# Performance work log

Hardware: AMD Instinct MI355X
Metric: run time of the kernel (lower is better)

The kernel has to match this reference:

```python
import jax, jax.numpy as jnp
import numpy as np

N_NODES = 50000
N_EDGES = 800000
N_GRAPHS = 64
NEG_SLOPE = 0.2  # PyG GATv2Conv default negative_slope
LN_EPS = 1e-5


def gatv2(x, src, dst, Wl, bl, Wr, br, att, bias, heads, out_ch, concat):
    """Faithful eval-mode PyG GATv2Conv: x_l=lin_l(x) (source), x_r=lin_r(x) (target),
    e = att . leaky_relu(x_l[src] + x_r[dst]), segment-softmax over dst, scatter-add."""
    N = x.shape[0]
    H, C = heads, out_ch
    xl = (x @ Wl + bl).reshape(N, H, C)
    xr = (x @ Wr + br).reshape(N, H, C)
    e = jax.nn.leaky_relu(xl[src] + xr[dst], NEG_SLOPE)        # [E, H, C]
    logits = jnp.einsum('ehc,hc->eh', e, att)                  # [E, H]
    m = jax.ops.segment_max(logits, dst, num_segments=N)       # every node has a self-loop
    ex = jnp.exp(logits - m[dst])
    denom = jax.ops.segment_sum(ex, dst, num_segments=N)
    alpha = ex / (denom[dst] + 1e-16)                          # [E, H]
    out = jax.ops.segment_sum(xl[src] * alpha[..., None], dst, num_segments=N)  # [N, H, C]
    out = out.reshape(N, H * C) if concat else out.mean(axis=1)
    return out + bias


def setup_inputs() -> dict:
    key = jax.random.key(0)
    ks = jax.random.split(key, 32)

    def g(i, shape):  # glorot-ish
        scale = np.sqrt(2.0 / (shape[0] + shape[-1]))
        return (jax.random.normal(ks[i], shape, jnp.float32) * scale)

    inp = {
        'x': jax.random.normal(ks[0], (N_NODES, 4), jnp.float32),
        'edge_index': jax.random.randint(ks[1], (2, N_EDGES), 0, N_NODES, dtype=jnp.int64),
        'batch': jnp.sort(jax.random.randint(ks[2], (N_NODES,), 0, N_GRAPHS, dtype=jnp.int64)),
        # conv1: 4 -> 64, heads=4, concat -> 256
        'W1l': g(3, (4, 256)), 'b1l': jnp.zeros((256,), jnp.float32),
        'W1r': g(4, (4, 256)), 'b1r': jnp.zeros((256,), jnp.float32),
        'a1': g(5, (4, 64)), 'c1b': jnp.zeros((256,), jnp.float32),
        # conv2: 256 -> 64, heads=2, concat -> 128
        'W2l': g(6, (256, 128)), 'b2l': jnp.zeros((128,), jnp.float32),
        'W2r': g(7, (256, 128)), 'b2r': jnp.zeros((128,), jnp.float32),
        'a2': g(8, (2, 64)), 'c2b': jnp.zeros((128,), jnp.float32),
        # conv3: 128 -> 256, heads=1, concat=False -> 256
        'W3l': g(9, (128, 256)), 'b3l': jnp.zeros((256,), jnp.float32),
        'W3r': g(10, (128, 256)), 'b3r': jnp.zeros((256,), jnp.float32),
        'a3': g(11, (1, 256)), 'c3b': jnp.zeros((256,), jnp.float32),
        # enhancer MLP + LayerNorm
        'We1': g(12, (256, 512)), 'be1': jnp.zeros((512,), jnp.float32),
        'We2': g(13, (512, 256)), 'be2': jnp.zeros((256,), jnp.float32),
        'lng': jnp.ones((256,), jnp.float32), 'lnb': jnp.zeros((256,), jnp.float32),
    }
    return inp


def reference(x, edge_index, batch,
              W1l, b1l, W1r, b1r, a1, c1b,
              W2l, b2l, W2r, b2r, a2, c2b,
              W3l, b3l, W3r, b3r, a3, c3b,
              We1, be1, We2, be2, lng, lnb):
    N = x.shape[0]
    loop = jnp.arange(N, dtype=edge_index.dtype)  # add_self_loops=True (PyG default)
    src = jnp.concatenate([edge_index[0], loop])
    dst = jnp.concatenate([edge_index[1], loop])

    h = jax.nn.relu(gatv2(x, src, dst, W1l, b1l, W1r, b1r, a1, c1b, 4, 64, True))
    h = jax.nn.relu(gatv2(h, src, dst, W2l, b2l, W2r, b2r, a2, c2b, 2, 64, True))
    h = gatv2(h, src, dst, W3l, b3l, W3r, b3r, a3, c3b, 1, 256, False)

    # global mean pool per graph
    sums = jax.ops.segment_sum(h, batch, num_segments=N_GRAPHS)          # [G, 256]
    cnt = jax.ops.segment_sum(jnp.ones((N, 1), h.dtype), batch, num_segments=N_GRAPHS)
    pooled = sums / jnp.maximum(cnt, 1.0)

    # enhancer (dropout off in eval): Linear -> ReLU -> Linear -> LayerNorm
    z = jax.nn.relu(pooled @ We1 + be1) @ We2 + be2
    mu = z.mean(axis=-1, keepdims=True)
    var = z.var(axis=-1, keepdims=True)
    return (z - mu) / jnp.sqrt(var + LN_EPS) * lng + lnb
```

## Files before the change

kernel.cpp:

```cpp
#include <hip/hip_runtime.h>
#include <hip/hip_bf16.h>
#include <math.h>

#define NN 50000
#define NE0 800000
#define ETOT (NE0 + NN)
#define NG 64
#define SCAN_BLKS ((NN + 63) / 64)
#define DMAX_THR 8.0f

typedef _Float16 h2 __attribute__((ext_vector_type(2)));
typedef _Float16 h8 __attribute__((ext_vector_type(8)));
typedef float    f32x4 __attribute__((ext_vector_type(4)));
typedef unsigned short us8 __attribute__((ext_vector_type(8)));

__device__ __forceinline__ unsigned short f2h(float f) {
    _Float16 h = (_Float16)f;
    return __builtin_bit_cast(unsigned short, h);
}
__device__ __forceinline__ float h2f(unsigned short u) {
    return (float)__builtin_bit_cast(_Float16, u);
}

__device__ __forceinline__ void edge_sd(const int* __restrict__ ei, int e, int& s, int& d) {
    if (e < NE0) { s = ei[e]; d = ei[NE0 + e]; }
    else { s = e - NE0; d = s; }
}

__global__ __launch_bounds__(256)
void hist_dst(const int* __restrict__ ei, int* __restrict__ deg) {
    int e = blockIdx.x * blockDim.x + threadIdx.x;
    if (e >= ETOT) return;
    int s, d; edge_sd(ei, e, s, d); (void)s;
    atomicAdd(&deg[d], 1);
}

__global__ __launch_bounds__(64)
void scan1(const int* __restrict__ deg, int* __restrict__ psum) {
    int i = blockIdx.x * 64 + threadIdx.x;
    int v = (i < NN) ? deg[i] : 0;
#pragma unroll
    for (int off = 1; off < 64; off <<= 1) {
        int t = __shfl_up(v, off);
        if ((int)threadIdx.x >= off) v += t;
    }
    if (threadIdx.x == 63) psum[blockIdx.x] = v;
}

__global__ __launch_bounds__(1024)
void scan2(int* __restrict__ psum) {
    __shared__ int sm[1024];
    int t = threadIdx.x;
    sm[t] = (t < SCAN_BLKS) ? psum[t] : 0;
    __syncthreads();
    for (int off = 1; off < 1024; off <<= 1) {
        int v = (t >= off) ? sm[t - off] : 0;
        __syncthreads();
        sm[t] += v;
        __syncthreads();
    }
    if (t < SCAN_BLKS) psum[t] = (t == 0) ? 0 : sm[t - 1];
}

__global__ __launch_bounds__(64)
void scan3(const int* __restrict__ deg, const int* __restrict__ psum,
           int* __restrict__ rowptr, int* __restrict__ cursor) {
    int i = blockIdx.x * 64 + threadIdx.x;
    int v = (i < NN) ? deg[i] : 0;
    int inc = v;
#pragma unroll
    for (int off = 1; off < 64; off <<= 1) {
        int t = __shfl_up(inc, off);
        if ((int)threadIdx.x >= off) inc += t;
    }
    int excl = inc - v + psum[blockIdx.x];
    if (i < NN) { rowptr[i] = excl; cursor[i] = excl; }
    if (i == NN - 1) rowptr[NN] = excl + v;
}

__global__ __launch_bounds__(256)
void scatter_csr(const int* __restrict__ ei, int* __restrict__ cursor,
                 int* __restrict__ col) {
    int e = blockIdx.x * blockDim.x + threadIdx.x;
    if (e >= ETOT) return;
    int s, d; edge_sd(ei, e, s, d);
    int pos = atomicAdd(&cursor[d], 1);
    col[pos] = s;
}

__device__ __forceinline__ void wfrag_one(const float* W, unsigned short* Wf,
                                          int r, int KB, int NOUT) {
    int j = r & 7;
    int l = (r >> 3) & 63;
    int rest = r >> 9;
    int kb = rest % KB, t = rest / KB;
    int k = kb * 32 + (l >> 4) * 8 + j;
    int colj = t * 16 + (l & 15);
    Wf[r] = f2h(W[(size_t)k * NOUT + colj]);
}
__global__ __launch_bounds__(256)
void wfrag_all(const float* __restrict__ W2l, const float* __restrict__ W2r,
               const float* __restrict__ W3l, const float* __restrict__ W3r,
               unsigned short* __restrict__ Wf2l, unsigned short* __restrict__ Wf2r,
               unsigned short* __restrict__ Wf3l, unsigned short* __restrict__ Wf3r,
               int* __restrict__ deg) {
    int tid = blockIdx.x * 256 + threadIdx.x;
    if (tid < NN) deg[tid] = 0;
    int seg = tid >> 15;
    int r = tid & 32767;
    if (seg == 0)      wfrag_one(W2l, Wf2l, r, 8, 128);
    else if (seg == 1) wfrag_one(W2r, Wf2r, r, 8, 128);
    else if (seg == 2) wfrag_one(W3l, Wf3l, r, 4, 256);
    else               wfrag_one(W3r, Wf3r, r, 4, 256);
}

__global__ __launch_bounds__(256)
void qr_prep(const float* __restrict__ X,
             const float* __restrict__ W1l, const float* __restrict__ b1l,
             const float* __restrict__ W1r, const float* __restrict__ b1r,
             unsigned short* __restrict__ Q, unsigned short* __restrict__ R) {
    int j = blockIdx.x * 64 + (threadIdx.x & 63);
    int row0 = (blockIdx.y * 4 + (threadIdx.x >> 6)) * 8;
    float l0 = W1l[j], l1 = W1l[256 + j], l2 = W1l[512 + j], l3 = W1l[768 + j];
    float r0 = W1r[j], r1 = W1r[256 + j], r2 = W1r[512 + j], r3 = W1r[768 + j];
    float bl = b1l[j], br = b1r[j];
#pragma unroll
    for (int r = 0; r < 8; ++r) {
        int row = row0 + r;
        if (row >= NN) break;
        float4 xv = *reinterpret_cast<const float4*>(X + (size_t)row * 4);
        float q = fmaf(xv.x, l0, fmaf(xv.y, l1, fmaf(xv.z, l2, fmaf(xv.w, l3, bl))));
        float rr = fmaf(xv.x, r0, fmaf(xv.y, r1, fmaf(xv.z, r2, fmaf(xv.w, r3, br))));
        Q[(size_t)row * 256 + j] = f2h(q);
        R[(size_t)row * 256 + j] = f2h(rr);
    }
}

template<int CPL, int REDW, bool RELU>
__global__ __launch_bounds__(256)
void gat_fused(const unsigned short* __restrict__ xl, const unsigned short* __restrict__ xr,
               const int* __restrict__ rowptr, const int* __restrict__ col,
               const float* __restrict__ att, const float* __restrict__ bias,
               unsigned short* __restrict__ out) {
    constexpr int HC = CPL * 32;
    constexpr int NP = CPL / 2;
    int lane = threadIdx.x & 63;
    int half = lane >> 5;
    int node = (blockIdx.x * blockDim.x + threadIdx.x) >> 6;
    if (node >= NN) return;
    int ch0 = (lane & 31) * CPL;

    const h2 c02 = (h2){(_Float16)0.2f, (_Float16)0.2f};
    h2 a2[NP];
#pragma unroll
    for (int p = 0; p < NP; ++p)
        a2[p] = (h2){(_Float16)att[ch0 + 2*p], (_Float16)att[ch0 + 2*p + 1]};
    h2 r2[NP];
    {
        const h2* rp = reinterpret_cast<const h2*>(xr + (size_t)node * HC + ch0);
#pragma unroll
        for (int p = 0; p < NP; ++p) r2[p] = rp[p];
    }

    float m = -INFINITY, l = 0.f, acc[CPL];
#pragma unroll
    for (int p = 0; p < CPL; ++p) acc[p] = 0.f;

    int beg = rowptr[node], end = rowptr[node + 1];
    int n = end - beg;
    int nh = (n + 1) >> 1;
    int idx = beg + (half ? nh : 0);
    int myEnd = half ? end : beg + nh;

    for (; idx + 3 < myEnd; idx += 4) {
        int s[4] = { col[idx], col[idx + 1], col[idx + 2], col[idx + 3] };
        h2 e[4][NP];
#pragma unroll
        for (int q = 0; q < 4; ++q) {
            const h2* pq = reinterpret_cast<const h2*>(xl + (size_t)s[q] * HC + ch0);
#pragma unroll
            for (int p = 0; p < NP; ++p) e[q][p] = pq[p];
        }
        float d[4] = { 0.f, 0.f, 0.f, 0.f };
#pragma unroll
        for (int p = 0; p < NP; ++p) {
#pragma unroll
            for (int q = 0; q < 4; ++q) {
                h2 u = e[q][p] + r2[p];
                u = __builtin_elementwise_max(u, u * c02);
                d[q] = __builtin_amdgcn_fdot2(u, a2[p], d[q], false);
            }
        }
#pragma unroll
        for (int off = REDW >> 1; off >= 1; off >>= 1) {
#pragma unroll
            for (int q = 0; q < 4; ++q) d[q] += __shfl_xor(d[q], off);
        }
        float pmax = fmaxf(fmaxf(d[0], d[1]), fmaxf(d[2], d[3]));
        if (pmax > m + DMAX_THR) {
            float sc = __expf(m - pmax);
            l *= sc;
#pragma unroll
            for (int p = 0; p < CPL; ++p) acc[p] *= sc;
            m = pmax;
        }
        float pw[4];
#pragma unroll
        for (int q = 0; q < 4; ++q) pw[q] = __expf(d[q] - m);
        l += (pw[0] + pw[1]) + (pw[2] + pw[3]);
#pragma unroll
        for (int p = 0; p < CPL; ++p) {
            float t0 = fmaf(pw[0], (float)e[0][p >> 1][p & 1],
                            pw[1] * (float)e[1][p >> 1][p & 1]);
            float t1 = fmaf(pw[2], (float)e[2][p >> 1][p & 1],
                            pw[3] * (float)e[3][p >> 1][p & 1]);
            acc[p] += t0 + t1;
        }
    }
    for (; idx < myEnd; ++idx) {
        int s0 = col[idx];
        const h2* p0 = reinterpret_cast<const h2*>(xl + (size_t)s0 * HC + ch0);
        h2 e0[NP];
#pragma unroll
        for (int p = 0; p < NP; ++p) e0[p] = p0[p];
        float d0 = 0.f;
#pragma unroll
        for (int p = 0; p < NP; ++p) {
            h2 u0 = e0[p] + r2[p];
            u0 = __builtin_elementwise_max(u0, u0 * c02);
            d0 = __builtin_amdgcn_fdot2(u0, a2[p], d0, false);
        }
#pragma unroll
        for (int off = REDW >> 1; off >= 1; off >>= 1) d0 += __shfl_xor(d0, off);
        if (d0 > m + DMAX_THR) {
            float sc = __expf(m - d0);
            l *= sc;
#pragma unroll
            for (int p = 0; p < CPL; ++p) acc[p] *= sc;
            m = d0;
        }
        float pw0 = __expf(d0 - m);
        l += pw0;
#pragma unroll
        for (int p = 0; p < CPL; ++p)
            acc[p] = fmaf(pw0, (float)e0[p >> 1][p & 1], acc[p]);
    }

    float mo = __shfl_xor(m, 32);
    float lo = __shfl_xor(l, 32);
    float M = fmaxf(m, mo);
    float sA = __expf(m - M), sB = __expf(mo - M);
    float lsum = l * sA + lo * sB;
    float inv = 1.f / (lsum + 1e-16f);
    unsigned short o[CPL];
#pragma unroll
    for (int p = 0; p < CPL; ++p) {
        float ao = __shfl_xor(acc[p], 32);
        float v = (acc[p] * sA + ao * sB) * inv + bias[ch0 + p];
        if (RELU) v = fmaxf(v, 0.f);
        o[p] = f2h(v);
    }
    if (half == 0) {
        if constexpr (CPL == 8) {
            us8 ov;
#pragma unroll
            for (int p = 0; p < 8; ++p) ov[p] = o[p];
            *reinterpret_cast<us8*>(out + (size_t)node * HC + ch0) = ov;
        } else {
            *reinterpret_cast<ushort4*>(out + (size_t)node * HC + ch0) =
                make_ushort4(o[0], o[1], o[2], o[3]);
        }
    }
}

template<int KIN, int NOUT>
__global__ __launch_bounds__(256)
void gemm_mfma2(const unsigned short* __restrict__ X,
                const unsigned short* __restrict__ WfL, const float* __restrict__ bL,
                unsigned short* __restrict__ outL,
                const unsigned short* __restrict__ WfR, const float* __restrict__ bR,
                unsigned short* __restrict__ outR) {
    constexpr int KB = KIN / 32, NT = NOUT / 16;
    int lane = threadIdx.x & 63;
    int wv = threadIdx.x >> 6;
    int row0 = blockIdx.x * 64 + wv * 16;
    int r16 = lane & 15, kg = lane >> 4;

    int arow = row0 + r16; if (arow >= NN) arow = NN - 1;
    const unsigned short* xrow = X + (size_t)arow * KIN + kg * 8;
    h8 af[KB];
#pragma unroll
    for (int kb = 0; kb < KB; ++kb)
        af[kb] = *reinterpret_cast<const h8*>(xrow + kb * 32);

    const unsigned short* Wf[2] = { WfL, WfR };
    const float* bb[2] = { bL, bR };
    unsigned short* oo[2] = { outL, outR };

#pragma unroll
    for (int w = 0; w < 2; ++w) {
        const h8* wbase = reinterpret_cast<const h8*>(Wf[w]) + lane;
        const float* bw = bb[w];
        unsigned short* ow = oo[w];
#pragma unroll 1
        for (int t = 0; t < NT; ++t) {
            f32x4 acc = {0.f, 0.f, 0.f, 0.f};
            const h8* wp = wbase + (size_t)t * KB * 64;
#pragma unroll
            for (int kb = 0; kb < KB; ++kb)
                acc = __builtin_amdgcn_mfma_f32_16x16x32_f16(af[kb], wp[kb * 64], acc, 0, 0, 0);
            float bv = bw[t * 16 + r16];
#pragma unroll
            for (int rg = 0; rg < 4; ++rg) {
                int row = row0 + kg * 4 + rg;
                if (row < NN)
                    ow[(size_t)row * NOUT + t * 16 + r16] = f2h(acc[rg] + bv);
            }
        }
    }
}

__global__ __launch_bounds__(256)
void graph_bounds(const int* __restrict__ batch, float* __restrict__ cnt,
                  float* __restrict__ pooled) {
    int g = blockIdx.x, tid = threadIdx.x;
    pooled[g * 256 + tid] = 0.f;
    if (tid == 0) {
        int lo = 0, hi = NN;
        while (lo < hi) { int mid = (lo + hi) >> 1; if (batch[mid] < g) lo = mid + 1; else hi = mid; }
        int lo2 = lo, hi2 = NN;
        while (lo2 < hi2) { int mid = (lo2 + hi2) >> 1; if (batch[mid] < g + 1) lo2 = mid + 1; else hi2 = mid; }
        cnt[g] = (float)(lo2 - lo);
    }
}

__global__ __launch_bounds__(256)
void pool_sum(const unsigned short* __restrict__ h, const int* __restrict__ batch,
              float* pooled) {
    __shared__ int gb[32];
    int c = threadIdx.x;
    int n0 = blockIdx.x * 32;
    int n1 = min(n0 + 32, NN);
    int cnt = n1 - n0;
    if (c < cnt) gb[c] = batch[n0 + c];
    __syncthreads();
    if (gb[0] == gb[cnt - 1]) {
        float acc = 0.f;
#pragma unroll 4
        for (int i = 0; i < cnt; ++i) acc += h2f(h[(size_t)(n0 + i) * 256 + c]);
        atomicAdd(&pooled[gb[0] * 256 + c], acc);
    } else {
        int cur = gb[0]; float acc = 0.f;
        for (int i = 0; i < cnt; ++i) {
            int g = gb[i];
            if (g != cur) { atomicAdd(&pooled[cur * 256 + c], acc); acc = 0.f; cur = g; }
            acc += h2f(h[(size_t)(n0 + i) * 256 + c]);
        }
        atomicAdd(&pooled[cur * 256 + c], acc);
    }
}

__global__ __launch_bounds__(256)
void mlp_ln(const float* __restrict__ pooled, const float* __restrict__ cnt,
            const float* __restrict__ We1, const float* __restrict__ be1,
            const float* __restrict__ We2, const float* __restrict__ be2,
            const float* __restrict__ lng, const float* __restrict__ lnb,
            float* __restrict__ out) {
    __shared__ float p[256];
    __shared__ float t[512];
    __shared__ float red[8];
    int g = blockIdx.x, tid = threadIdx.x;
    p[tid] = pooled[g * 256 + tid] / fmaxf(cnt[g], 1.0f);
    __syncthreads();
    for (int jj = tid; jj < 512; jj += 256) {
        float s = be1[jj];
        for (int k = 0; k < 256; ++k) s = fmaf(p[k], We1[(size_t)k * 512 + jj], s);
        t[jj] = fmaxf(s, 0.f);
    }
    __syncthreads();
    float z = be2[tid];
    for (int k = 0; k < 512; ++k) z = fmaf(t[k], We2[(size_t)k * 256 + tid], z);
    float sv = z, sq = z * z;
#pragma unroll
    for (int off = 32; off >= 1; off >>= 1) {
        sv += __shfl_xor(sv, off);
        sq += __shfl_xor(sq, off);
    }
    int wv = tid >> 6;
    if ((tid & 63) == 0) { red[wv] = sv; red[4 + wv] = sq; }
    __syncthreads();
    float tot = red[0] + red[1] + red[2] + red[3];
    float totq = red[4] + red[5] + red[6] + red[7];
    float mu = tot * (1.f / 256.f);
    float var = totq * (1.f / 256.f) - mu * mu;
    float r = rsqrtf(var + 1e-5f);
    out[g * 256 + tid] = (z - mu) * r * lng[tid] + lnb[tid];
}

extern "C" void kernel_launch(void* const* d_in, const int* in_sizes, int n_in,
                              void* d_out, int out_size, void* d_ws, size_t ws_size,
                              hipStream_t stream) {
    const float* x   = (const float*)d_in[0];
    const int*   ei  = (const int*)d_in[1];
    const int*   bat = (const int*)d_in[2];
    const float *W1l = (const float*)d_in[3], *b1l = (const float*)d_in[4];
    const float *W1r = (const float*)d_in[5], *b1r = (const float*)d_in[6];
    const float *a1  = (const float*)d_in[7], *c1b = (const float*)d_in[8];
    const float *W2l = (const float*)d_in[9],  *b2l = (const float*)d_in[10];
    const float *W2r = (const float*)d_in[11], *b2r = (const float*)d_in[12];
    const float *a2  = (const float*)d_in[13], *c2b = (const float*)d_in[14];
    const float *W3l = (const float*)d_in[15], *b3l = (const float*)d_in[16];
    const float *W3r = (const float*)d_in[17], *b3r = (const float*)d_in[18];
    const float *a3  = (const float*)d_in[19], *c3b = (const float*)d_in[20];
    const float *We1 = (const float*)d_in[21], *be1 = (const float*)d_in[22];
    const float *We2 = (const float*)d_in[23], *be2 = (const float*)d_in[24];
    const float *lng = (const float*)d_in[25], *lnb = (const float*)d_in[26];

    char* base = (char*)d_ws;
    size_t off = 0;
    auto nxt = [&](size_t bytes) { char* p = base + off; off = (off + bytes + 255) & ~(size_t)255; return p; };
    unsigned short* Abuf = (unsigned short*)nxt((size_t)NN * 256 * 2);
    unsigned short* Bbuf = (unsigned short*)nxt((size_t)NN * 256 * 2);
    unsigned short* Hb16 = (unsigned short*)nxt((size_t)NN * 256 * 2);
    unsigned short* Qtab = (unsigned short*)nxt((size_t)NN * 256 * 2);
    unsigned short* Rtab = (unsigned short*)nxt((size_t)NN * 256 * 2);
    int* deg    = (int*)nxt(NN * 4);
    int* rowptr = (int*)nxt((NN + 1) * 4);
    int* cursor = (int*)nxt(NN * 4);
    int* colv   = (int*)nxt((size_t)ETOT * 4);
    int* psum   = (int*)nxt(1024 * 4);
    float* POOL = (float*)nxt(NG * 256 * 4);
    float* CNT  = (float*)nxt(NG * 4);
    unsigned short* Wf2l = (unsigned short*)nxt(256 * 128 * 2);
    unsigned short* Wf2r = (unsigned short*)nxt(256 * 128 * 2);
    unsigned short* Wf3l = (unsigned short*)nxt(128 * 256 * 2);
    unsigned short* Wf3r = (unsigned short*)nxt(128 * 256 * 2);

    const int GEMM_BLKS = (NN + 63) / 64;
    const int NB_NODE = (NN + 3) / 4;

    wfrag_all<<<(4 * 32768) / 256, 256, 0, stream>>>(W2l, W2r, W3l, W3r,
                                                     Wf2l, Wf2r, Wf3l, Wf3r, deg);
    hist_dst<<<(ETOT + 255) / 256, 256, 0, stream>>>(ei, deg);
    scan1<<<SCAN_BLKS, 64, 0, stream>>>(deg, psum);
    scan2<<<1, 1024, 0, stream>>>(psum);
    scan3<<<SCAN_BLKS, 64, 0, stream>>>(deg, psum, rowptr, cursor);
    scatter_csr<<<(ETOT + 255) / 256, 256, 0, stream>>>(ei, cursor, colv);

    {
        dim3 g(4, (NN + 31) / 32);
        qr_prep<<<g, 256, 0, stream>>>(x, W1l, b1l, W1r, b1r, Qtab, Rtab);
    }

    gat_fused<8, 8, true><<<NB_NODE, 256, 0, stream>>>(Qtab, Rtab, rowptr, colv, a1, c1b, Hb16);

    gemm_mfma2<256, 128><<<GEMM_BLKS, 256, 0, stream>>>(Hb16, Wf2l, b2l, Abuf, Wf2r, b2r, Bbuf);
    gat_fused<4, 16, true><<<NB_NODE, 256, 0, stream>>>(Abuf, Bbuf, rowptr, colv, a2, c2b, Hb16);

    gemm_mfma2<128, 256><<<GEMM_BLKS, 256, 0, stream>>>(Hb16, Wf3l, b3l, Abuf, Wf3r, b3r, Bbuf);
    gat_fused<8, 32, false><<<NB_NODE, 256, 0, stream>>>(Abuf, Bbuf, rowptr, colv, a3, c3b, Hb16);

    graph_bounds<<<NG, 256, 0, stream>>>(bat, CNT, POOL);
    pool_sum<<<(NN + 31) / 32, 256, 0, stream>>>(Hb16, bat, POOL);
    mlp_ln<<<NG, 256, 0, stream>>>(POOL, CNT, We1, be1, We2, be2, lng, lnb, (float*)d_out);
}
```

Measured before the change: 413.4 us.

## Accumulate GAT messages in packed fp16 and generalize edge split per node

The fused GAT kernel now keeps the weighted-message accumulator in packed half2 registers and updates it with packed fp16 multiply-adds, replacing per-channel fp32 FMAs. It also generalizes the per-node edge split from two groups to a template SPLIT with a tree merge of partial softmax states. Layer 2 now uses 4 groups of 16 lanes with 8 channels each. The rescale threshold drops from 8 to 4 to limit fp16 overflow. Together these aim to cut ALU and register cost and add edge-level parallelism, at the cost of fp16 accumulation error and extra shuffles in the merge.

```diff
diff --git a/kernel.cpp b/kernel.cpp
--- a/kernel.cpp
+++ b/kernel.cpp
@@ -7,7 +7,7 @@
 #define ETOT (NE0 + NN)
 #define NG 64
 #define SCAN_BLKS ((NN + 63) / 64)
-#define DMAX_THR 8.0f
+#define DMAX_THR 4.0f
 
 typedef _Float16 h2 __attribute__((ext_vector_type(2)));
 typedef _Float16 h8 __attribute__((ext_vector_type(8)));
@@ -20,6 +20,10 @@
 }
 __device__ __forceinline__ float h2f(unsigned short u) {
     return (float)__builtin_bit_cast(_Float16, u);
+}
+__device__ __forceinline__ h2 shfl_h2(h2 v, int off) {
+    int x = __builtin_bit_cast(int, v);
+    return __builtin_bit_cast(h2, __shfl_xor(x, off));
 }
 
 __device__ __forceinline__ void edge_sd(const int* __restrict__ ei, int e, int& s, int& d) {
@@ -136,19 +140,21 @@
     }
 }
 
-template<int CPL, int REDW, bool RELU>
+template<int CPL, int REDW, int SPLIT, bool RELU>
 __global__ __launch_bounds__(256)
 void gat_fused(const unsigned short* __restrict__ xl, const unsigned short* __restrict__ xr,
                const int* __restrict__ rowptr, const int* __restrict__ col,
                const float* __restrict__ att, const float* __restrict__ bias,
                unsigned short* __restrict__ out) {
-    constexpr int HC = CPL * 32;
+    constexpr int GL = 64 / SPLIT;
+    constexpr int HC = CPL * GL;
     constexpr int NP = CPL / 2;
     int lane = threadIdx.x & 63;
-    int half = lane >> 5;
+    int grp = lane / GL;
+    int gl = lane & (GL - 1);
     int node = (blockIdx.x * blockDim.x + threadIdx.x) >> 6;
     if (node >= NN) return;
-    int ch0 = (lane & 31) * CPL;
+    int ch0 = gl * CPL;
 
     const h2 c02 = (h2){(_Float16)0.2f, (_Float16)0.2f};
     h2 a2[NP];
@@ -162,15 +168,16 @@
         for (int p = 0; p < NP; ++p) r2[p] = rp[p];
     }
 
-    float m = -INFINITY, l = 0.f, acc[CPL];
-#pragma unroll
-    for (int p = 0; p < CPL; ++p) acc[p] = 0.f;
+    float m = -INFINITY, l = 0.f;
+    h2 acch[NP];
+#pragma unroll
+    for (int p = 0; p < NP; ++p) acch[p] = (h2){(_Float16)0.f, (_Float16)0.f};
 
     int beg = rowptr[node], end = rowptr[node + 1];
     int n = end - beg;
-    int nh = (n + 1) >> 1;
-    int idx = beg + (half ? nh : 0);
-    int myEnd = half ? end : beg + nh;
+    int per = (n + SPLIT - 1) / SPLIT;
+    int idx = beg + grp * per; if (idx > end) idx = end;
+    int myEnd = idx + per; if (myEnd > end) myEnd = end;
 
     for (; idx + 3 < myEnd; idx += 4) {
         int s[4] = { col[idx], col[idx + 1], col[idx + 2], col[idx + 3] };
@@ -199,22 +206,28 @@
         float pmax = fmaxf(fmaxf(d[0], d[1]), fmaxf(d[2], d[3]));
         if (pmax > m + DMAX_THR) {
             float sc = __expf(m - pmax);
+            h2 sch = (h2){(_Float16)sc, (_Float16)sc};
             l *= sc;
 #pragma unroll
-            for (int p = 0; p < CPL; ++p) acc[p] *= sc;
+            for (int p = 0; p < NP; ++p) acch[p] *= sch;
             m = pmax;
         }
         float pw[4];
 #pragma unroll
         for (int q = 0; q < 4; ++q) pw[q] = __expf(d[q] - m);
         l += (pw[0] + pw[1]) + (pw[2] + pw[3]);
-#pragma unroll
-        for (int p = 0; p < CPL; ++p) {
-            float t0 = fmaf(pw[0], (float)e[0][p >> 1][p & 1],
-                            pw[1] * (float)e[1][p >> 1][p & 1]);
-            float t1 = fmaf(pw[2], (float)e[2][p >> 1][p & 1],
-                            pw[3] * (float)e[3][p >> 1][p & 1]);
-            acc[p] += t0 + t1;
+        h2 pg[4];
+#pragma unroll
+        for (int q = 0; q < 4; ++q)
+            pg[q] = (h2){(_Float16)pw[q], (_Float16)pw[q]};
+#pragma unroll
+        for (int p = 0; p < NP; ++p) {
+            h2 a = acch[p];
+            a += pg[0] * e[0][p];
+            a += pg[1] * e[1][p];
+            a += pg[2] * e[2][p];
+            a += pg[3] * e[3][p];
+            acch[p] = a;
         }
     }
     for (; idx < myEnd; ++idx) {
@@ -234,33 +247,47 @@
         for (int off = REDW >> 1; off >= 1; off >>= 1) d0 += __shfl_xor(d0, off);
         if (d0 > m + DMAX_THR) {
             float sc = __expf(m - d0);
+            h2 sch = (h2){(_Float16)sc, (_Float16)sc};
             l *= sc;
 #pragma unroll
-            for (int p = 0; p < CPL; ++p) acc[p] *= sc;
+            for (int p = 0; p < NP; ++p) acch[p] *= sch;
             m = d0;
         }
         float pw0 = __expf(d0 - m);
         l += pw0;
-#pragma unroll
-        for (int p = 0; p < CPL; ++p)
-            acc[p] = fmaf(pw0, (float)e0[p >> 1][p & 1], acc[p]);
-    }
-
-    float mo = __shfl_xor(m, 32);
-    float lo = __shfl_xor(l, 32);
-    float M = fmaxf(m, mo);
-    float sA = __expf(m - M), sB = __expf(mo - M);
-    float lsum = l * sA + lo * sB;
-    float inv = 1.f / (lsum + 1e-16f);
+        h2 pg = (h2){(_Float16)pw0, (_Float16)pw0};
+#pragma unroll
+        for (int p = 0; p < NP; ++p)
+            acch[p] += pg * e0[p];
+    }
+
+#pragma unroll
+    for (int stage = GL; stage < 64; stage <<= 1) {
+        float mo = __shfl_xor(m, stage);
+        float lo = __shfl_xor(l, stage);
+        float M = fmaxf(m, mo);
+        float sA = (m > -INFINITY) ? __expf(m - M) : 0.f;
+        float sB = (mo > -INFINITY) ? __expf(mo - M) : 0.f;
+        l = l * sA + lo * sB;
+        h2 sAh = (h2){(_Float16)sA, (_Float16)sA};
+        h2 sBh = (h2){(_Float16)sB, (_Float16)sB};
+#pragma unroll
+        for (int p = 0; p < NP; ++p) {
+            h2 ao = shfl_h2(acch[p], stage);
+            acch[p] = acch[p] * sAh + ao * sBh;
+        }
+        m = M;
+    }
+
+    float inv = 1.f / (l + 1e-16f);
     unsigned short o[CPL];
 #pragma unroll
     for (int p = 0; p < CPL; ++p) {
-        float ao = __shfl_xor(acc[p], 32);
-        float v = (acc[p] * sA + ao * sB) * inv + bias[ch0 + p];
+        float v = (float)acch[p >> 1][p & 1] * inv + bias[ch0 + p];
         if (RELU) v = fmaxf(v, 0.f);
         o[p] = f2h(v);
     }
-    if (half == 0) {
+    if (grp == 0) {
         if constexpr (CPL == 8) {
             us8 ov;
 #pragma unroll
@@ -452,13 +479,13 @@
         qr_prep<<<g, 256, 0, stream>>>(x, W1l, b1l, W1r, b1r, Qtab, Rtab);
     }
 
-    gat_fused<8, 8, true><<<NB_NODE, 256, 0, stream>>>(Qtab, Rtab, rowptr, colv, a1, c1b, Hb16);
+    gat_fused<8, 8, 2, true><<<NB_NODE, 256, 0, stream>>>(Qtab, Rtab, rowptr, colv, a1, c1b, Hb16);
 
     gemm_mfma2<256, 128><<<GEMM_BLKS, 256, 0, stream>>>(Hb16, Wf2l, b2l, Abuf, Wf2r, b2r, Bbuf);
-    gat_fused<4, 16, true><<<NB_NODE, 256, 0, stream>>>(Abuf, Bbuf, rowptr, colv, a2, c2b, Hb16);
+    gat_fused<8, 8, 4, true><<<NB_NODE, 256, 0, stream>>>(Abuf, Bbuf, rowptr, colv, a2, c2b, Hb16);
 
     gemm_mfma2<128, 256><<<GEMM_BLKS, 256, 0, stream>>>(Hb16, Wf3l, b3l, Abuf, Wf3r, b3r, Bbuf);
-    gat_fused<8, 32, false><<<NB_NODE, 256, 0, stream>>>(Abuf, Bbuf, rowptr, colv, a3, c3b, Hb16);
+    gat_fused<8, 32, 2, false><<<NB_NODE, 256, 0, stream>>>(Abuf, Bbuf, rowptr, colv, a3, c3b, Hb16);
 
     graph_bounds<<<NG, 256, 0, stream>>>(bat, CNT, POOL);
     pool_sum<<<(NN + 31) / 32, 256, 0, stream>>>(Hb16, bat, POOL);
```

Measured after the change: 412.1 us. Within noise of the previous version (-0.3%).
